# Kernel optimization log

Hardware: AMD Instinct MI355X
Metric: run time of the kernel (lower is better)

Reference implementation:

```python
import jax, jax.numpy as jnp
import numpy as np

B, S, H, NH, HD, V = 2, 2048, 1024, 16, 64, 32000
BASE = 10000.0
NEG = jnp.finfo(jnp.float32).min


def setup_inputs() -> dict:
    key = jax.random.key(0)
    ks = jax.random.split(key, 12)
    batch = jax.random.randint(ks[0], (B, S), 0, V)
    positions = jnp.broadcast_to(jnp.arange(S), (B, S))
    lengths = jax.random.randint(ks[1], (B,), 1, S + 1)  # >=1 to avoid fully-masked rows
    sc = 1.0 / np.sqrt(H)
    emb = jax.random.normal(ks[2], (V, H), dtype=jnp.float32) * 0.02
    wq = jax.random.normal(ks[3], (H, NH * HD), dtype=jnp.float32) * sc
    bq = jnp.zeros((NH * HD,), jnp.float32)
    wk = jax.random.normal(ks[4], (H, NH * HD), dtype=jnp.float32) * sc
    bk = jnp.zeros((NH * HD,), jnp.float32)
    wv = jax.random.normal(ks[5], (H, NH * HD), dtype=jnp.float32) * sc
    bv = jnp.zeros((NH * HD,), jnp.float32)
    wo = jax.random.normal(ks[6], (NH * HD, H), dtype=jnp.float32) * sc
    bo = jnp.zeros((H,), jnp.float32)
    return dict(batch=batch, positions=positions, lengths=lengths, emb=emb,
                wq=wq, bq=bq, wk=wk, bk=bk, wv=wv, bv=bv, wo=wo, bo=bo)


def _rope(x, positions):
    # x: [B, NH, S, HD]; positions: [B, S] int
    inv_freq = 1.0 / (BASE ** (jnp.arange(0, HD, 2, dtype=jnp.float32) / HD))  # [HD/2]
    freqs = positions.astype(jnp.float32)[..., None] * inv_freq               # [B, S, HD/2]
    ang = jnp.concatenate([freqs, freqs], axis=-1)                            # [B, S, HD]
    cos = jnp.cos(ang)[:, None]                                               # [B, 1, S, HD]
    sin = jnp.sin(ang)[:, None]
    x1, x2 = x[..., :HD // 2], x[..., HD // 2:]
    rot = jnp.concatenate([-x2, x1], axis=-1)
    return x * cos + rot * sin


def reference(batch, positions, lengths, emb, wq, bq, wk, bk, wv, bv, wo, bo):
    h = emb[batch]                                                 # [B, S, H]
    q = (h @ wq + bq).reshape(B, S, NH, HD).transpose(0, 2, 1, 3)  # [B, NH, S, HD]
    k = (h @ wk + bk).reshape(B, S, NH, HD).transpose(0, 2, 1, 3)
    v = (h @ wv + bv).reshape(B, S, NH, HD).transpose(0, 2, 1, 3)
    q = _rope(q, positions)
    k = _rope(k, positions)
    scores = jnp.einsum('bhqd,bhkd->bhqk', q, k) / np.sqrt(HD)     # [B, NH, S, S]
    causal = jnp.triu(jnp.full((S, S), NEG, jnp.float32), 1)
    pad = jnp.where(jnp.arange(S)[None, :] < lengths[:, None], 0.0, NEG)  # [B, S]
    mask = pad[:, None, None, :] + causal[None, None]              # [B, 1, S, S]
    attn = jax.nn.softmax(scores + mask, axis=-1)
    out = jnp.einsum('bhqk,bhkd->bhqd', attn, v)                   # [B, NH, S, HD]
    out = out.transpose(0, 2, 1, 3).reshape(B, S, NH * HD)
    return out @ wo + bo                                           # [B, S, H]
```

## Files before the change

### kernel.cpp

```cpp
#include <hip/hip_runtime.h>
#include <hip/hip_bf16.h>
#include <cstdint>

#define DEVINL __device__ __forceinline__

typedef __attribute__((ext_vector_type(8))) short short8;
typedef __attribute__((ext_vector_type(4))) float f32x4;

constexpr int B_ = 2, S_ = 2048, H_ = 1024, NH_ = 16, HD_ = 64;
constexpr int M_ = B_ * S_;
constexpr float SC2 = 0.18033688f;

DEVINL float bf2f(unsigned short h) {
    unsigned u = ((unsigned)h) << 16;
    float f; __builtin_memcpy(&f, &u, 4); return f;
}
DEVINL unsigned short f2bf(float f) {
    unsigned u; __builtin_memcpy(&u, &f, 4);
    u += 0x7FFFu + ((u >> 16) & 1u);
    return (unsigned short)(u >> 16);
}
DEVINL unsigned pk2bf(float a, float b) {
    __hip_bfloat162 h = __float22bfloat162_rn(float2{a, b});
    unsigned u; __builtin_memcpy(&u, &h, 4); return u;
}
DEVINL float fexp2(float x) {
#if __has_builtin(__builtin_amdgcn_exp2f)
    return __builtin_amdgcn_exp2f(x);
#else
    return exp2f(x);
#endif
}
DEVINL float ldin(const void* p, size_t i, int fp32) {
    return fp32 ? ((const float*)p)[i] : bf2f(((const unsigned short*)p)[i]);
}
DEVINL void gl16(const void* g, void* l) {
    __builtin_amdgcn_global_load_lds(
        (const __attribute__((address_space(1))) unsigned int*)g,
        (__attribute__((address_space(3))) unsigned int*)l, 16, 0, 0);
}
DEVINL f32x4 mfma16(short8 a, short8 b, f32x4 c) {
    return __builtin_amdgcn_mfma_f32_16x16x32_bf16(a, b, c, 0, 0, 0);
}
DEVINL void fsincos(float rev01, float* sn, float* cs) {
#if __has_builtin(__builtin_amdgcn_sinf) && __has_builtin(__builtin_amdgcn_cosf)
    *sn = __builtin_amdgcn_sinf(rev01);
    *cs = __builtin_amdgcn_cosf(rev01);
#else
    float a = rev01 * 6.28318530717958647692f;
    *sn = __sinf(a); *cs = __cosf(a);
#endif
}
DEVINL int detect_fp32(const unsigned short* emb, int t) {
    unsigned short hw = emb[2 * t];
    unsigned e = (hw >> 7) & 0xFFu;
    int s = (((e >= 90u) && (e <= 126u)) || ((hw & 0x7FFFu) == 0u)) ? 1 : 0;
    #pragma unroll
    for (int o = 1; o < 64; o <<= 1) s += __shfl_xor(s, o);
    __shared__ int cnt[4];
    if ((t & 63) == 0) cnt[t >> 6] = s;
    __syncthreads();
    return ((cnt[0] + cnt[1] + cnt[2] + cnt[3]) > 192) ? 0 : 1;
}

__global__ __launch_bounds__(256) void k_prep(const void* w0, const void* w1,
                                              const void* w2, const void* w3,
                                              const void* bq, const void* bk,
                                              const void* bv, const void* bo,
                                              const unsigned short* __restrict__ emb,
                                              const int* __restrict__ batch,
                                              int* __restrict__ flag,
                                              float* __restrict__ biasws,
                                              unsigned short* __restrict__ wT,
                                              unsigned short* __restrict__ hbuf) {
    int tx = threadIdx.x, ty = threadIdx.y, t = ty * 32 + tx;
    int fp32 = detect_fp32(emb, t);
    int z = blockIdx.z;
    if (z == 4) {
        if (!fp32) return;
        int g = blockIdx.y * 32 + blockIdx.x;
        int w = t >> 6, lane = t & 63;
        int row = g * 4 + w;
        int tok = batch[row];
        const float4* s = (const float4*)((const float*)emb + (size_t)tok * H_);
        unsigned long long* d = (unsigned long long*)(hbuf + (size_t)row * H_);
        #pragma unroll
        for (int c = 0; c < 4; c++) {
            float4 x = s[lane + 64 * c];
            d[lane + 64 * c] = (unsigned long long)f2bf(x.x)
                             | ((unsigned long long)f2bf(x.y) << 16)
                             | ((unsigned long long)f2bf(x.z) << 32)
                             | ((unsigned long long)f2bf(x.w) << 48);
        }
        return;
    }
    __shared__ float tile[32][33];
    int mat = z;
    if (mat == 0 && blockIdx.y == 0) {
        if (blockIdx.x == 0 && t == 0) flag[0] = fp32;
        if (blockIdx.x < 16) {
            int i = blockIdx.x * 256 + t;
            const void* src = (i < 1024) ? bq : (i < 2048) ? bk : (i < 3072) ? bv : bo;
            biasws[i] = ldin(src, (size_t)(i & 1023), fp32);
        }
    }
    const void* w = (mat == 0) ? w0 : (mat == 1) ? w1 : (mat == 2) ? w2 : w3;
    int n0 = blockIdx.x * 32, k0 = blockIdx.y * 32;
    for (int i = ty; i < 32; i += 8)
        tile[i][tx] = ldin(w, (size_t)(k0 + i) * 1024 + n0 + tx, fp32);
    __syncthreads();
    unsigned short* dst = wT + (size_t)mat * 1024 * 1024;
    for (int i = ty; i < 32; i += 8)
        dst[(size_t)(n0 + i) * 1024 + k0 + tx] = f2bf(tile[tx][i]);
}

__global__ __launch_bounds__(256) void k_gemm_qkv(const unsigned short* __restrict__ embb,
                                                  const unsigned short* __restrict__ hbuf,
                                                  const int* __restrict__ batch,
                                                  const unsigned short* __restrict__ Bt,
                                                  const float* __restrict__ bias,
                                                  const int* __restrict__ positions,
                                                  const int* __restrict__ flag,
                                                  unsigned short* __restrict__ qo,
                                                  unsigned short* __restrict__ ko,
                                                  unsigned short* __restrict__ vt) {
    constexpr int K = 1024;
    __shared__ alignas(16) unsigned short As[2][128 * 32];
    __shared__ alignas(16) unsigned short Bs[2][128 * 32];
    int t = threadIdx.x, lane = t & 63, quad = lane >> 4, n16 = lane & 15;
    int w = t >> 6, wm = w >> 1, wn = w & 1;
    int m0 = blockIdx.y * 128, n0 = blockIdx.x * 128;
    int fp32 = flag[0];
    int r0 = t >> 2, r1 = 64 + r0;
    int ka = (t & 3) * 8;
    const unsigned short* a0;
    const unsigned short* a1;
    if (fp32) {
        a0 = hbuf + (size_t)(m0 + r0) * K;
        a1 = hbuf + (size_t)(m0 + r1) * K;
    } else {
        a0 = embb + (size_t)batch[m0 + r0] * K;
        a1 = embb + (size_t)batch[m0 + r1] * K;
    }
    const unsigned short* b0 = Bt + (size_t)(n0 + r0) * K;
    const unsigned short* b1 = Bt + (size_t)(n0 + r1) * K;
    f32x4 acc[4][4];
    #pragma unroll
    for (int mi = 0; mi < 4; mi++)
        #pragma unroll
        for (int ni = 0; ni < 4; ni++) acc[mi][ni] = (f32x4){0.f, 0.f, 0.f, 0.f};
    for (int k0 = 0; k0 < K; k0 += 64) {
        __syncthreads();
        gl16(a0 + k0 + ka,      &As[0][t * 8]);
        gl16(a1 + k0 + ka,      &As[0][(t + 256) * 8]);
        gl16(a0 + k0 + 32 + ka, &As[1][t * 8]);
        gl16(a1 + k0 + 32 + ka, &As[1][(t + 256) * 8]);
        gl16(b0 + k0 + ka,      &Bs[0][t * 8]);
        gl16(b1 + k0 + ka,      &Bs[0][(t + 256) * 8]);
        gl16(b0 + k0 + 32 + ka, &Bs[1][t * 8]);
        gl16(b1 + k0 + 32 + ka, &Bs[1][(t + 256) * 8]);
        __syncthreads();
        #pragma unroll
        for (int ks = 0; ks < 2; ks++) {
            short8 af[4], bfr[4];
            #pragma unroll
            for (int mi = 0; mi < 4; mi++)
                af[mi] = *(const short8*)&As[ks][(wm * 64 + mi * 16 + n16) * 32 + quad * 8];
            #pragma unroll
            for (int ni = 0; ni < 4; ni++)
                bfr[ni] = *(const short8*)&Bs[ks][(wn * 64 + ni * 16 + n16) * 32 + quad * 8];
            #pragma unroll
            for (int mi = 0; mi < 4; mi++)
                #pragma unroll
                for (int ni = 0; ni < 4; ni++)
                    acc[mi][ni] = mfma16(af[mi], bfr[ni], acc[mi][ni]);
        }
    }
    int colbase = n0 + wn * 64;
    int buf = colbase >> 10;
    int cc = colbase & 1023;
    float bb[4];
    #pragma unroll
    for (int ni = 0; ni < 4; ni++) bb[ni] = bias[colbase + ni * 16 + n16];
    if (buf == 2) {
        #pragma unroll
        for (int mi = 0; mi < 4; mi++) {
            int row = m0 + wm * 64 + mi * 16 + quad * 4;
            int bb_ = row >> 11;
            int s0 = row & 2047;
            int pos = (s0 & ~31) + quad * 8 + (mi & 1) * 4;
            #pragma unroll
            for (int ni = 0; ni < 4; ni++) {
                int f = cc + ni * 16 + n16;
                unsigned long long pk =
                      (unsigned long long)pk2bf(acc[mi][ni][0] + bb[ni], acc[mi][ni][1] + bb[ni])
                    | ((unsigned long long)pk2bf(acc[mi][ni][2] + bb[ni], acc[mi][ni][3] + bb[ni]) << 32);
                *(unsigned long long*)(vt + ((size_t)(bb_ * 1024 + f)) * 2048 + pos) = pk;
            }
        }
    } else {
        unsigned short* out = (buf == 0) ? qo : ko;
        float osc = (buf == 0) ? SC2 : 1.0f;
        float revf[2];
        #pragma unroll
        for (int ni = 0; ni < 2; ni++) {
            float d = (float)(ni * 16 + n16);
            revf[ni] = __expf(d * -0.28782313f) * 0.15915494f;
        }
        #pragma unroll
        for (int mi = 0; mi < 4; mi++) {
            int row0 = m0 + wm * 64 + mi * 16 + quad * 4;
            #pragma unroll
            for (int i = 0; i < 4; i++) {
                int row = row0 + i;
                float pos = (float)positions[row];
                #pragma unroll
                for (int ni = 0; ni < 2; ni++) {
                    float rev = pos * revf[ni];
                    float fr = rev - floorf(rev);
                    float sn, cs; fsincos(fr, &sn, &cs);
                    float x1 = (acc[mi][ni][i] + bb[ni]) * osc;
                    float x2 = (acc[mi][ni + 2][i] + bb[ni + 2]) * osc;
                    out[(size_t)row * 1024 + cc + ni * 16 + n16] = f2bf(x1 * cs - x2 * sn);
                    out[(size_t)row * 1024 + cc + (ni + 2) * 16 + n16] = f2bf(x2 * cs + x1 * sn);
                }
            }
        }
    }
}

__global__ __launch_bounds__(256) void k_attn(const unsigned short* __restrict__ q,
                                              const unsigned short* __restrict__ k_,
                                              const unsigned short* __restrict__ vt,
                                              const int* __restrict__ lengths,
                                              unsigned short* __restrict__ o) {
    __shared__ alignas(16) unsigned short Ks[2][64 * 64];
    __shared__ alignas(16) unsigned short Vs[2][64 * 64];
    int bx = blockIdx.x;
    int traw = bx & 31, hh = (bx >> 5) & 15, b = bx >> 9;
    int tile = ((bx >> 8) & 1) ? (31 - traw) : traw;
    int t = threadIdx.x, w = t >> 6, lane = t & 63, quad = lane >> 4, n16 = lane & 15;
    int len = lengths[b];
    int kend = min(tile * 64 + 64, len);
    int nkt = (kend + 63) >> 6;
    int qrow = tile * 64 + w * 16 + n16;
    int limit = min(qrow, len - 1);
    int tbw = tile * 64 + w * 16;
    short8 qf[2];
    {
        size_t qa = ((size_t)(b * S_ + qrow)) * H_ + hh * 64 + quad * 8;
        qf[0] = *(const short8*)(q + qa);
        qf[1] = *(const short8*)(q + qa + 32);
    }
    f32x4 oa[4];
    float l_ = 0.f;
    #pragma unroll
    for (int nb = 0; nb < 4; nb++) oa[nb] = (f32x4){0.f, 0.f, 0.f, 0.f};
    const unsigned short* kbase = k_ + ((size_t)b * S_) * H_ + hh * 64;
    const unsigned short* vbase = vt + ((size_t)(b * 1024 + hh * 64)) * 2048;
    int sr0 = t >> 3, sc0 = (t & 7) ^ (sr0 & 7);
    int sr1 = (t + 256) >> 3, sc1 = (t & 7) ^ (sr1 & 7);
    auto stage = [&](int kt) {
        int kb = kt * 64, bi = kt & 1;
        gl16(kbase + (size_t)(kb + sr0) * H_ + sc0 * 8, &Ks[bi][t * 8]);
        gl16(kbase + (size_t)(kb + sr1) * H_ + sc1 * 8, &Ks[bi][(t + 256) * 8]);
        gl16(vbase + (size_t)sr0 * 2048 + kb + sc0 * 8, &Vs[bi][t * 8]);
        gl16(vbase + (size_t)sr1 * 2048 + kb + sc1 * 8, &Vs[bi][(t + 256) * 8]);
    };
    stage(0);
    for (int kt = 0; kt < nkt; kt++) {
        int kb = kt * 64, bi = kt & 1;
        __syncthreads();
        if (kt + 1 < nkt) stage(kt + 1);
        const unsigned short* Kb = Ks[bi];
        const unsigned short* Vb = Vs[bi];
        short8 kf[4][2];
        #pragma unroll
        for (int st = 0; st < 4; st++)
            #pragma unroll
            for (int hf = 0; hf < 2; hf++) {
                int ky = st * 16 + n16;
                kf[st][hf] = *(const short8*)&Kb[ky * 64 + (((hf * 4 + quad) ^ (ky & 7)) * 8)];
            }
        f32x4 sc[4];
        #pragma unroll
        for (int st = 0; st < 4; st++) {
            f32x4 z = (f32x4){0.f, 0.f, 0.f, 0.f};
            z = mfma16(kf[st][0], qf[0], z);
            z = mfma16(kf[st][1], qf[1], z);
            sc[st] = z;
        }
        float rs = 0.f;
        if (kb + 64 <= min(tbw, len)) {
            #pragma unroll
            for (int st = 0; st < 4; st++)
                #pragma unroll
                for (int i = 0; i < 4; i++) {
                    float p = fexp2(sc[st][i]);
                    rs += p;
                    sc[st][i] = p;
                }
        } else {
            #pragma unroll
            for (int st = 0; st < 4; st++)
                #pragma unroll
                for (int i = 0; i < 4; i++) {
                    int kg = kb + st * 16 + quad * 4 + i;
                    float p = (kg <= limit) ? fexp2(sc[st][i]) : 0.f;
                    rs += p;
                    sc[st][i] = p;
                }
        }
        rs += __shfl_xor(rs, 16);
        rs += __shfl_xor(rs, 32);
        l_ += rs;
        short8 vf[2][4];
        #pragma unroll
        for (int p = 0; p < 2; p++)
            #pragma unroll
            for (int nb = 0; nb < 4; nb++) {
                int f = nb * 16 + n16;
                vf[p][nb] = *(const short8*)&Vb[f * 64 + (((p * 4 + quad) ^ (f & 7)) * 8)];
            }
        #pragma unroll
        for (int p = 0; p < 2; p++) {
            union { unsigned u[4]; short8 v8; } pp;
            pp.u[0] = pk2bf(sc[2 * p][0], sc[2 * p][1]);
            pp.u[1] = pk2bf(sc[2 * p][2], sc[2 * p][3]);
            pp.u[2] = pk2bf(sc[2 * p + 1][0], sc[2 * p + 1][1]);
            pp.u[3] = pk2bf(sc[2 * p + 1][2], sc[2 * p + 1][3]);
            #pragma unroll
            for (int nb = 0; nb < 4; nb++)
                oa[nb] = mfma16(pp.v8, vf[p][nb], oa[nb]);
        }
    }
    f32x4 rl;
    #pragma unroll
    for (int i = 0; i < 4; i++) rl[i] = 1.f / __shfl(l_, quad * 4 + i);
    #pragma unroll
    for (int nb = 0; nb < 4; nb++) {
        #pragma unroll
        for (int i = 0; i < 4; i++) {
            int row = tile * 64 + w * 16 + quad * 4 + i;
            o[((size_t)(b * S_ + row)) * H_ + hh * 64 + nb * 16 + n16] =
                f2bf(oa[nb][i] * rl[i]);
        }
    }
}

__global__ __launch_bounds__(256) void k_gemm64(const unsigned short* __restrict__ A,
                                                const unsigned short* __restrict__ Bt,
                                                const float* __restrict__ bias,
                                                unsigned short* __restrict__ Cb,
                                                float* __restrict__ Cf,
                                                const int* __restrict__ flag) {
    constexpr int K = 1024, N = 1024;
    __shared__ alignas(16) unsigned short As[2][64 * 32];
    __shared__ alignas(16) unsigned short Bs[2][128 * 32];
    int t = threadIdx.x, lane = t & 63, quad = lane >> 4, n16 = lane & 15;
    int w = t >> 6, wm = w & 1, wn = w >> 1;
    int m0 = blockIdx.y * 64, n0 = blockIdx.x * 128;
    int r0 = t >> 2, r1 = 64 + r0, ka = (t & 3) * 8;
    const unsigned short* a0 = A + (size_t)(m0 + r0) * K;
    const unsigned short* b0 = Bt + (size_t)(n0 + r0) * K;
    const unsigned short* b1 = Bt + (size_t)(n0 + r1) * K;
    f32x4 acc[2][4];
    #pragma unroll
    for (int mi = 0; mi < 2; mi++)
        #pragma unroll
        for (int ni = 0; ni < 4; ni++) acc[mi][ni] = (f32x4){0.f, 0.f, 0.f, 0.f};
    for (int k0 = 0; k0 < K; k0 += 64) {
        __syncthreads();
        gl16(a0 + k0 + ka,      &As[0][t * 8]);
        gl16(a0 + k0 + 32 + ka, &As[1][t * 8]);
        gl16(b0 + k0 + ka,      &Bs[0][t * 8]);
        gl16(b1 + k0 + ka,      &Bs[0][(t + 256) * 8]);
        gl16(b0 + k0 + 32 + ka, &Bs[1][t * 8]);
        gl16(b1 + k0 + 32 + ka, &Bs[1][(t + 256) * 8]);
        __syncthreads();
        #pragma unroll
        for (int ks = 0; ks < 2; ks++) {
            short8 af[2], bfr[4];
            #pragma unroll
            for (int mi = 0; mi < 2; mi++)
                af[mi] = *(const short8*)&As[ks][(wm * 32 + mi * 16 + n16) * 32 + quad * 8];
            #pragma unroll
            for (int ni = 0; ni < 4; ni++)
                bfr[ni] = *(const short8*)&Bs[ks][(wn * 64 + ni * 16 + n16) * 32 + quad * 8];
            #pragma unroll
            for (int mi = 0; mi < 2; mi++)
                #pragma unroll
                for (int ni = 0; ni < 4; ni++)
                    acc[mi][ni] = mfma16(af[mi], bfr[ni], acc[mi][ni]);
        }
    }
    int fp32out = (flag[0] == 1);
    #pragma unroll
    for (int mi = 0; mi < 2; mi++) {
        #pragma unroll
        for (int ni = 0; ni < 4; ni++) {
            int row = m0 + wm * 32 + mi * 16 + quad * 4;
            int col = n0 + wn * 64 + ni * 16 + n16;
            float bb = bias[col];
            #pragma unroll
            for (int i = 0; i < 4; i++) {
                float val = acc[mi][ni][i] + bb;
                size_t idx = (size_t)(row + i) * N + col;
                if (fp32out) Cf[idx] = val;
                else         Cb[idx] = f2bf(val);
            }
        }
    }
}

extern "C" void kernel_launch(void* const* d_in, const int* in_sizes, int n_in,
                              void* d_out, int out_size, void* d_ws, size_t ws_size,
                              hipStream_t stream) {
    (void)in_sizes; (void)n_in; (void)out_size; (void)ws_size;
    const int* batch     = (const int*)d_in[0];
    const int* positions = (const int*)d_in[1];
    const int* lengths   = (const int*)d_in[2];
    const void* emb = d_in[3];
    const void* wq = d_in[4];  const void* bq = d_in[5];
    const void* wk = d_in[6];  const void* bk = d_in[7];
    const void* wv = d_in[8];  const void* bv = d_in[9];
    const void* wo = d_in[10]; const void* bo = d_in[11];

    char* ws = (char*)d_ws;
    int*   flag   = (int*)ws;
    float* biasws = (float*)(ws + 4096);
    unsigned short* wT = (unsigned short*)(ws + 20480);
    size_t off = 20480 + (8ull << 20);
    unsigned short* hbuf = (unsigned short*)(ws + off); off += (8ull << 20);
    unsigned short* qb   = (unsigned short*)(ws + off); off += (8ull << 20);
    unsigned short* kb2  = (unsigned short*)(ws + off); off += (8ull << 20);
    unsigned short* vtb  = (unsigned short*)(ws + off); off += (8ull << 20);
    unsigned short* ao   = (unsigned short*)(ws + off); off += (8ull << 20);

    k_prep<<<dim3(32, 32, 5), dim3(32, 8), 0, stream>>>(
        wq, wk, wv, wo, bq, bk, bv, bo, (const unsigned short*)emb, batch,
        flag, biasws, wT, hbuf);

    k_gemm_qkv<<<dim3(3072 / 128, M_ / 128), 256, 0, stream>>>(
        (const unsigned short*)emb, hbuf, batch, wT, biasws, positions, flag,
        qb, kb2, vtb);

    k_attn<<<B_ * NH_ * 32, 256, 0, stream>>>(qb, kb2, vtb, lengths, ao);

    k_gemm64<<<dim3(1024 / 128, M_ / 64), 256, 0, stream>>>(
        ao, wT + (3ull << 20), biasws + 3072,
        (unsigned short*)d_out, (float*)d_out, flag);
}
```

Measured before the change: 300.4 us.

## Restructure QKV GEMM into 256x256 tiles with double-buffered LDS pipeline

The QKV projection GEMM moves from 128x128 tiles with 256 threads to 256x256 tiles with 512 threads (8 waves). Global-to-LDS loads for the next K-step are issued while the current step computes, using ping-pong LDS buffers. An XOR swizzle reduces LDS bank conflicts, and the block index is remapped so neighbouring blocks share tiles in L2. The compute is split into four MFMA phases separated by raw barriers with setprio, which makes the code more complex and uses far more LDS (128KB) and registers. The larger tiles also leave a smaller grid.

```diff
diff --git a/kernel.cpp b/kernel.cpp
--- a/kernel.cpp
+++ b/kernel.cpp
@@ -50,6 +50,11 @@
     float a = rev01 * 6.28318530717958647692f;
     *sn = __sinf(a); *cs = __cosf(a);
 #endif
+}
+DEVINL void barrier_raw() {
+    asm volatile("" ::: "memory");
+    __builtin_amdgcn_s_barrier();
+    asm volatile("" ::: "memory");
 }
 DEVINL int detect_fp32(const unsigned short* emb, int t) {
     unsigned short hw = emb[2 * t];
@@ -114,67 +119,133 @@
         dst[(size_t)(n0 + i) * 1024 + k0 + tx] = f2bf(tile[tx][i]);
 }
 
-__global__ __launch_bounds__(256) void k_gemm_qkv(const unsigned short* __restrict__ embb,
-                                                  const unsigned short* __restrict__ hbuf,
-                                                  const int* __restrict__ batch,
-                                                  const unsigned short* __restrict__ Bt,
-                                                  const float* __restrict__ bias,
-                                                  const int* __restrict__ positions,
-                                                  const int* __restrict__ flag,
-                                                  unsigned short* __restrict__ qo,
-                                                  unsigned short* __restrict__ ko,
-                                                  unsigned short* __restrict__ vt) {
-    constexpr int K = 1024;
-    __shared__ alignas(16) unsigned short As[2][128 * 32];
-    __shared__ alignas(16) unsigned short Bs[2][128 * 32];
+__global__ __launch_bounds__(512, 2) void k_gemm_qkv(const unsigned short* __restrict__ embb,
+                                                     const unsigned short* __restrict__ hbuf,
+                                                     const int* __restrict__ batch,
+                                                     const unsigned short* __restrict__ Bt,
+                                                     const float* __restrict__ bias,
+                                                     const int* __restrict__ positions,
+                                                     const int* __restrict__ flag,
+                                                     unsigned short* __restrict__ qo,
+                                                     unsigned short* __restrict__ ko,
+                                                     unsigned short* __restrict__ vt) {
+    constexpr int K = 1024, NT = 16;
+    __shared__ alignas(16) unsigned short L[2][2][16384];
     int t = threadIdx.x, lane = t & 63, quad = lane >> 4, n16 = lane & 15;
-    int w = t >> 6, wm = w >> 1, wn = w & 1;
-    int m0 = blockIdx.y * 128, n0 = blockIdx.x * 128;
+    int w = t >> 6, wm = w >> 2, wn = w & 3;
+    int id = blockIdx.y * 12 + blockIdx.x;
+    int sw = (id & 7) * 24 + (id >> 3);
+    int m0 = (sw / 12) * 256, n0 = (sw % 12) * 256;
     int fp32 = flag[0];
-    int r0 = t >> 2, r1 = 64 + r0;
-    int ka = (t & 3) * 8;
-    const unsigned short* a0;
-    const unsigned short* a1;
-    if (fp32) {
-        a0 = hbuf + (size_t)(m0 + r0) * K;
-        a1 = hbuf + (size_t)(m0 + r1) * K;
-    } else {
-        a0 = embb + (size_t)batch[m0 + r0] * K;
-        a1 = embb + (size_t)batch[m0 + r1] * K;
-    }
-    const unsigned short* b0 = Bt + (size_t)(n0 + r0) * K;
-    const unsigned short* b1 = Bt + (size_t)(n0 + r1) * K;
-    f32x4 acc[4][4];
-    #pragma unroll
-    for (int mi = 0; mi < 4; mi++)
+    int sr = t >> 3;
+    int colOff = ((t & 7) ^ (sr & 7)) * 8;
+    const unsigned short* aS[2][2];
+    const unsigned short* bS[2][2];
+    #pragma unroll
+    for (int h = 0; h < 2; h++)
+        #pragma unroll
+        for (int j = 0; j < 2; j++) {
+            int gR = m0 + h * 128 + j * 64 + sr;
+            aS[h][j] = fp32 ? hbuf + (size_t)gR * K
+                            : embb + (size_t)batch[gR] * K;
+            bS[h][j] = Bt + (size_t)(n0 + h * 128 + j * 64 + sr) * K;
+        }
+    int ldst = t * 8;
+    auto stage = [&](int kt) {
+        int s = kt & 1, k0 = kt * 64;
+        #pragma unroll
+        for (int h = 0; h < 2; h++)
+            #pragma unroll
+            for (int j = 0; j < 2; j++) {
+                gl16(aS[h][j] + k0 + colOff, &L[s][0][h * 8192 + j * 4096 + ldst]);
+                gl16(bS[h][j] + k0 + colOff, &L[s][1][h * 8192 + j * 4096 + ldst]);
+            }
+    };
+    f32x4 acc[8][4];
+    #pragma unroll
+    for (int mi = 0; mi < 8; mi++)
         #pragma unroll
         for (int ni = 0; ni < 4; ni++) acc[mi][ni] = (f32x4){0.f, 0.f, 0.f, 0.f};
-    for (int k0 = 0; k0 < K; k0 += 64) {
-        __syncthreads();
-        gl16(a0 + k0 + ka,      &As[0][t * 8]);
-        gl16(a1 + k0 + ka,      &As[0][(t + 256) * 8]);
-        gl16(a0 + k0 + 32 + ka, &As[1][t * 8]);
-        gl16(a1 + k0 + 32 + ka, &As[1][(t + 256) * 8]);
-        gl16(b0 + k0 + ka,      &Bs[0][t * 8]);
-        gl16(b1 + k0 + ka,      &Bs[0][(t + 256) * 8]);
-        gl16(b0 + k0 + 32 + ka, &Bs[1][t * 8]);
-        gl16(b1 + k0 + 32 + ka, &Bs[1][(t + 256) * 8]);
-        __syncthreads();
-        #pragma unroll
-        for (int ks = 0; ks < 2; ks++) {
-            short8 af[4], bfr[4];
-            #pragma unroll
-            for (int mi = 0; mi < 4; mi++)
-                af[mi] = *(const short8*)&As[ks][(wm * 64 + mi * 16 + n16) * 32 + quad * 8];
-            #pragma unroll
-            for (int ni = 0; ni < 4; ni++)
-                bfr[ni] = *(const short8*)&Bs[ks][(wn * 64 + ni * 16 + n16) * 32 + quad * 8];
-            #pragma unroll
-            for (int mi = 0; mi < 4; mi++)
-                #pragma unroll
-                for (int ni = 0; ni < 4; ni++)
-                    acc[mi][ni] = mfma16(af[mi], bfr[ni], acc[mi][ni]);
-        }
+    int x7 = n16 & 7;
+    int cs0 = (quad ^ x7) * 8;
+    int cs1 = ((4 + quad) ^ x7) * 8;
+    int aRow = n16 * 64;
+    int bRow = ((wn & 1) * 64 + n16) * 64;
+    stage(0);
+    asm volatile("s_waitcnt vmcnt(0)" ::: "memory");
+    barrier_raw();
+    for (int tt = 0; tt < NT; ++tt) {
+        int s = tt & 1;
+        const unsigned short* LA = &L[s][0][wm * 8192];
+        const unsigned short* LB = &L[s][1][(wn >> 1) * 8192];
+        short8 Af[4][2], Bf[2][2], Bg[2][2];
+        if (tt + 1 < NT) stage(tt + 1);
+        #pragma unroll
+        for (int mi = 0; mi < 4; mi++) {
+            Af[mi][0] = *(const short8*)&LA[aRow + mi * 1024 + cs0];
+            Af[mi][1] = *(const short8*)&LA[aRow + mi * 1024 + cs1];
+        }
+        #pragma unroll
+        for (int ni = 0; ni < 2; ni++) {
+            Bf[ni][0] = *(const short8*)&LB[bRow + ni * 1024 + cs0];
+            Bf[ni][1] = *(const short8*)&LB[bRow + ni * 1024 + cs1];
+        }
+        barrier_raw();
+        asm volatile("s_waitcnt lgkmcnt(0)" ::: "memory");
+        __builtin_amdgcn_sched_barrier(0);
+        __builtin_amdgcn_s_setprio(1);
+        #pragma unroll
+        for (int mi = 0; mi < 4; mi++)
+            #pragma unroll
+            for (int ni = 0; ni < 2; ni++)
+                acc[mi][ni] = mfma16(Af[mi][1], Bf[ni][1],
+                              mfma16(Af[mi][0], Bf[ni][0], acc[mi][ni]));
+        __builtin_amdgcn_s_setprio(0);
+        barrier_raw();
+        #pragma unroll
+        for (int ni = 0; ni < 2; ni++) {
+            Bg[ni][0] = *(const short8*)&LB[bRow + (ni + 2) * 1024 + cs0];
+            Bg[ni][1] = *(const short8*)&LB[bRow + (ni + 2) * 1024 + cs1];
+        }
+        barrier_raw();
+        asm volatile("s_waitcnt lgkmcnt(0)" ::: "memory");
+        __builtin_amdgcn_sched_barrier(0);
+        __builtin_amdgcn_s_setprio(1);
+        #pragma unroll
+        for (int mi = 0; mi < 4; mi++)
+            #pragma unroll
+            for (int ni = 0; ni < 2; ni++)
+                acc[mi][ni + 2] = mfma16(Af[mi][1], Bg[ni][1],
+                                  mfma16(Af[mi][0], Bg[ni][0], acc[mi][ni + 2]));
+        __builtin_amdgcn_s_setprio(0);
+        barrier_raw();
+        #pragma unroll
+        for (int mi = 0; mi < 4; mi++) {
+            Af[mi][0] = *(const short8*)&LA[aRow + (mi + 4) * 1024 + cs0];
+            Af[mi][1] = *(const short8*)&LA[aRow + (mi + 4) * 1024 + cs1];
+        }
+        barrier_raw();
+        asm volatile("s_waitcnt lgkmcnt(0)" ::: "memory");
+        __builtin_amdgcn_sched_barrier(0);
+        __builtin_amdgcn_s_setprio(1);
+        #pragma unroll
+        for (int mi = 0; mi < 4; mi++)
+            #pragma unroll
+            for (int ni = 0; ni < 2; ni++)
+                acc[mi + 4][ni] = mfma16(Af[mi][1], Bf[ni][1],
+                                  mfma16(Af[mi][0], Bf[ni][0], acc[mi + 4][ni]));
+        __builtin_amdgcn_s_setprio(0);
+        barrier_raw();
+        __builtin_amdgcn_s_setprio(1);
+        #pragma unroll
+        for (int mi = 0; mi < 4; mi++)
+            #pragma unroll
+            for (int ni = 0; ni < 2; ni++)
+                acc[mi + 4][ni + 2] = mfma16(Af[mi][1], Bg[ni][1],
+                                      mfma16(Af[mi][0], Bg[ni][0], acc[mi + 4][ni + 2]));
+        __builtin_amdgcn_s_setprio(0);
+        asm volatile("s_waitcnt vmcnt(0)" ::: "memory");
+        barrier_raw();
     }
     int colbase = n0 + wn * 64;
     int buf = colbase >> 10;
@@ -184,8 +255,8 @@
     for (int ni = 0; ni < 4; ni++) bb[ni] = bias[colbase + ni * 16 + n16];
     if (buf == 2) {
         #pragma unroll
-        for (int mi = 0; mi < 4; mi++) {
-            int row = m0 + wm * 64 + mi * 16 + quad * 4;
+        for (int mi = 0; mi < 8; mi++) {
+            int row = m0 + wm * 128 + mi * 16 + quad * 4;
             int bb_ = row >> 11;
             int s0 = row & 2047;
             int pos = (s0 & ~31) + quad * 8 + (mi & 1) * 4;
@@ -208,8 +279,8 @@
             revf[ni] = __expf(d * -0.28782313f) * 0.15915494f;
         }
         #pragma unroll
-        for (int mi = 0; mi < 4; mi++) {
-            int row0 = m0 + wm * 64 + mi * 16 + quad * 4;
+        for (int mi = 0; mi < 8; mi++) {
+            int row0 = m0 + wm * 128 + mi * 16 + quad * 4;
             #pragma unroll
             for (int i = 0; i < 4; i++) {
                 int row = row0 + i;
@@ -441,7 +512,7 @@
         wq, wk, wv, wo, bq, bk, bv, bo, (const unsigned short*)emb, batch,
         flag, biasws, wT, hbuf);
 
-    k_gemm_qkv<<<dim3(3072 / 128, M_ / 128), 256, 0, stream>>>(
+    k_gemm_qkv<<<dim3(12, 16), 512, 0, stream>>>(
         (const unsigned short*)emb, hbuf, batch, wT, biasws, positions, flag,
         qb, kb2, vtb);
 
```

Result: faster. 291.7 us (-2.9%).
